# Optimization experiments

Measured on AMD Instinct MI355X. Metric: run time of the kernel, lower is better.

The kernel has to match this reference:

```python
import jax, jax.numpy as jnp
import numpy as np

NUM_CATEGORIES = 72
TEMPERATURE = 0.07
SEGMENT_WEIGHT = 10.0
MISSING_CATEGORIES = (13, 53, 61)
EPS = 1e-12
NEG_INF = -1e30


def setup_inputs() -> dict:
    key = jax.random.key(0)
    k1, k2 = jax.random.split(key)
    B, N, D = 4, 262144, 32
    embeddings = jax.random.normal(k1, (B, N, D), dtype=jnp.float32)
    segment_labels = jax.random.randint(k2, (B, N), 0, NUM_CATEGORIES, dtype=jnp.int64)
    return {"embeddings": embeddings, "segment_labels": segment_labels}


def _l2norm(x):
    return x / jnp.maximum(jnp.linalg.norm(x, axis=-1, keepdims=True), EPS)


def reference(embeddings, segment_labels):
    C = NUM_CATEGORIES
    missing = jnp.zeros((C,), dtype=bool).at[jnp.array(MISSING_CATEGORIES)].set(True)
    valid = segment_labels >= 0                      # [B,N]
    labels = jnp.clip(segment_labels, 0, C - 1)      # safe indices
    emb_n = _l2norm(embeddings)                      # [B,N,D]

    def per_batch(e, lab, v):
        w = v.astype(e.dtype)                                        # [N]
        counts = jax.ops.segment_sum(w, lab, num_segments=C)         # [C]
        sums = jax.ops.segment_sum(e * w[:, None], lab, num_segments=C)  # [C,D]
        protos = _l2norm(sums / jnp.maximum(counts, 1.0)[:, None])   # [C,D]
        present = (counts > 0) & (~missing)                          # [C]
        # similarity over all categories, mask absent/missing prototypes
        sim = jnp.einsum('nd,cd->nc', e, protos) / TEMPERATURE       # [N,C]
        logits = jnp.where(present[None, :], sim, NEG_INF)
        logp = jax.nn.log_softmax(logits, axis=-1)
        nll = -jnp.take_along_axis(logp, lab[:, None], axis=1)[:, 0]  # [N]
        keep = (v & (~missing[lab])).astype(e.dtype)                  # ignore_index=-100 analogue
        return jnp.sum(nll * keep) / jnp.maximum(jnp.sum(keep), 1.0)

    losses = jax.vmap(per_batch)(emb_n, labels, valid)  # [B]
    segment_loss = jnp.mean(losses)                     # segment_count == B here
    return SEGMENT_WEIGHT * segment_loss
```

## Files before the change

kernel.cpp:

```cpp
#include <hip/hip_runtime.h>
#include <hip/hip_bf16.h>

#define NCAT 72
#define NCATP 80
#define DIM 32
#define BNUM 4
#define TEMP_INV (1.0f / 0.07f)
#define SEG_W 10.0f

#define WS_SUMS 0
#define WS_CNTS 9216
#define WS_PROT 9504
#define WS_NABS 19744
#define WS_LOSS 19748
#define WS_KEEP 19752
#define WS_TOTAL 19756

typedef __attribute__((ext_vector_type(8))) short short8v;
typedef __attribute__((ext_vector_type(4))) float f32x4;

__device__ __forceinline__ bool is_missing(int c) {
    return (c == 13) | (c == 53) | (c == 61);
}

__device__ __forceinline__ short f2bf_hi(float f, float* hi_f) {
    unsigned u = __float_as_uint(f);
    unsigned r = u + 0x7FFFu + ((u >> 16) & 1u);
    *hi_f = __uint_as_float(r & 0xFFFF0000u);
    return (short)(r >> 16);
}
__device__ __forceinline__ short f2bf(float f) {
    unsigned u = __float_as_uint(f);
    unsigned r = u + 0x7FFFu + ((u >> 16) & 1u);
    return (short)(r >> 16);
}

template <int BPB>
__global__ __launch_bounds__(256) void k_accum(const float* __restrict__ emb,
                                               const int* __restrict__ lab,
                                               float* __restrict__ ws, int Nb) {
    __shared__ float s_acc[4][NCAT][DIM];
    __shared__ float s_cnt[4][NCAT];
    const int t = threadIdx.x;
    const int b = blockIdx.x / BPB;
    const int blk = blockIdx.x % BPB;
    const int w = t >> 6;
    const int g = (t >> 3) & 7;
    const int sub = t & 7;
    const int pofs = t >> 3;

    for (int i = t; i < 4 * NCAT * DIM; i += 256) ((float*)s_acc)[i] = 0.f;
    for (int i = t; i < 4 * NCAT; i += 256) ((float*)s_cnt)[i] = 0.f;
    __syncthreads();

    float* accw = &s_acc[w][0][0];
    const float* eb = emb + (size_t)b * Nb * DIM;
    const int* lb = lab + (size_t)b * Nb;

    int p = blk * 32 + pofs;
    int l_cur = lb[p];
    float4 v_cur = ((const float4*)(eb + (size_t)p * DIM))[sub];

    for (int p0 = blk * 32; p0 < Nb; p0 += BPB * 32) {
        const int pn = p0 + BPB * 32 + pofs;
        int l_nxt = -1;
        float4 v_nxt = make_float4(0.f, 0.f, 0.f, 0.f);
        if (pn < Nb) {
            l_nxt = lb[pn];
            v_nxt = ((const float4*)(eb + (size_t)pn * DIM))[sub];
        }

        float ss = v_cur.x * v_cur.x + v_cur.y * v_cur.y +
                   v_cur.z * v_cur.z + v_cur.w * v_cur.w;
        ss += __shfl_xor(ss, 1);
        ss += __shfl_xor(ss, 2);
        ss += __shfl_xor(ss, 4);
        const float inv = 1.0f / fmaxf(sqrtf(ss), 1e-12f);
        const bool valid = (l_cur >= 0);
        const int lc = min(max(l_cur, 0), NCAT - 1);
        float4 u;
        u.x = v_cur.x * inv; u.y = v_cur.y * inv;
        u.z = v_cur.z * inv; u.w = v_cur.w * inv;

        if (valid && sub == 0) unsafeAtomicAdd(&s_cnt[w][lc], 1.0f);

        float* rowp = accw + lc * DIM + sub * 4;
        #pragma unroll
        for (int k = 0; k < 8; k++) {
            if (g == k && valid) {
                float4* r4 = (float4*)rowp;
                float4 o = *r4;
                o.x += u.x; o.y += u.y; o.z += u.z; o.w += u.w;
                *r4 = o;
            }
            __builtin_amdgcn_sched_barrier(0);
        }

        l_cur = l_nxt;
        v_cur = v_nxt;
    }
    __syncthreads();

    float* gs = ws + WS_SUMS + b * NCAT * DIM;
    const float* sa = (const float*)s_acc;
    for (int i = t; i < NCAT * DIM; i += 256) {
        float val = sa[i] + sa[NCAT * DIM + i] +
                    sa[2 * NCAT * DIM + i] + sa[3 * NCAT * DIM + i];
        if (val != 0.f) unsafeAtomicAdd(&gs[i], val);
    }
    if (t < NCAT) {
        float c = s_cnt[0][t] + s_cnt[1][t] + s_cnt[2][t] + s_cnt[3][t];
        if (c != 0.f) unsafeAtomicAdd(ws + WS_CNTS + b * NCAT + t, c);
    }
}

__global__ __launch_bounds__(256) void k_proto(float* __restrict__ ws) {
    const int b = blockIdx.x;
    __shared__ float s_np;
    if (threadIdx.x == 0) s_np = 0.f;
    __syncthreads();
    const float* gs = ws + WS_SUMS + b * NCAT * DIM;
    const float* gc = ws + WS_CNTS + b * NCAT;
    float* gp = ws + WS_PROT + b * NCATP * DIM;
    const int dd = threadIdx.x & 31;
    const int r0 = threadIdx.x >> 5;
    for (int c = r0; c < NCAT; c += 8) {
        float cnt = gc[c];
        float val = gs[c * DIM + dd] / fmaxf(cnt, 1.0f);
        float ss = val * val;
        #pragma unroll
        for (int m = 16; m >= 1; m >>= 1) ss += __shfl_xor(ss, m);
        float inv = 1.0f / fmaxf(sqrtf(ss), 1e-12f);
        const bool present = (cnt > 0.f) && !is_missing(c);
        gp[c * DIM + dd] = present ? val * inv : 0.f;
        if (dd == 0) unsafeAtomicAdd(&s_np, present ? 1.f : 0.f);
    }
    __syncthreads();
    if (threadIdx.x == 0) ws[WS_NABS + b] = (float)NCATP - s_np;
}

__device__ __forceinline__ void point_group(
    int pt, const float* __restrict__ eb, const int* __restrict__ lb,
    const float* __restrict__ pp, const short8v phi[5], const short8v plo[5],
    float nabs, int sub, float& lacc, float& kacc)
{
    const float LOG2E = 1.4426950408889634f;
    const int l = lb[pt];
    const int lc = min(max(l, 0), NCAT - 1);

    const float4* ep = (const float4*)(eb + (size_t)pt * DIM + sub * 8);
    float4 a0 = ep[0], a1 = ep[1];

    float ss = a0.x * a0.x + a0.y * a0.y + a0.z * a0.z + a0.w * a0.w +
               a1.x * a1.x + a1.y * a1.y + a1.z * a1.z + a1.w * a1.w;
    ss += __shfl_xor(ss, 16);
    ss += __shfl_xor(ss, 32);
    const float sca = (TEMP_INV * LOG2E) / fmaxf(sqrtf(ss), 1e-12f);
    a0.x *= sca; a0.y *= sca; a0.z *= sca; a0.w *= sca;
    a1.x *= sca; a1.y *= sca; a1.z *= sca; a1.w *= sca;

    const float4* qk = (const float4*)(pp + lc * DIM + sub * 8);
    float4 q0 = qk[0], q1 = qk[1];
    float dl = q0.x * a0.x + q0.y * a0.y + q0.z * a0.z + q0.w * a0.w +
               q1.x * a1.x + q1.y * a1.y + q1.z * a1.z + q1.w * a1.w;
    dl += __shfl_xor(dl, 16);
    dl += __shfl_xor(dl, 32);

    const bool keep = (l >= 0) && !is_missing(lc);

    float ea[8] = {a0.x, a0.y, a0.z, a0.w, a1.x, a1.y, a1.z, a1.w};
    short8v ehi, elo;
    #pragma unroll
    for (int j = 0; j < 8; j++) {
        float hf;
        ehi[j] = f2bf_hi(ea[j], &hf);
        elo[j] = f2bf(ea[j] - hf);
    }

    float s = 0.f;
    #pragma unroll
    for (int n = 0; n < 5; n++) {
        f32x4 acc = {0.f, 0.f, 0.f, 0.f};
        acc = __builtin_amdgcn_mfma_f32_16x16x32_bf16(phi[n], ehi, acc, 0, 0, 0);
        acc = __builtin_amdgcn_mfma_f32_16x16x32_bf16(plo[n], ehi, acc, 0, 0, 0);
        acc = __builtin_amdgcn_mfma_f32_16x16x32_bf16(phi[n], elo, acc, 0, 0, 0);
        s += __builtin_amdgcn_exp2f(acc[0]) + __builtin_amdgcn_exp2f(acc[1]) +
             __builtin_amdgcn_exp2f(acc[2]) + __builtin_amdgcn_exp2f(acc[3]);
    }
    s += __shfl_xor(s, 16);
    s += __shfl_xor(s, 32);
    s -= nabs;
    const float cl = __builtin_amdgcn_logf(s);
    if (keep && sub == 0) {
        lacc += cl - dl;
        kacc += 1.f;
    }
}

template <int BPB>
__global__ __launch_bounds__(256, 4) void k_loss(const float* __restrict__ emb,
                                                 const int* __restrict__ lab,
                                                 const float* __restrict__ protos,
                                                 const float* __restrict__ nabsp,
                                                 float* __restrict__ lossout,
                                                 int Nb) {
    __shared__ float s_red[8];
    const int b = blockIdx.x / BPB;
    const int blk = blockIdx.x % BPB;
    const int t = threadIdx.x;
    const int lane = t & 63;
    const int wave = t >> 6;
    const int lid = lane & 15;
    const int sub = lane >> 4;

    const float* pp = protos + b * NCATP * DIM;
    const float nabs = nabsp[b];
    const float* eb = emb + (size_t)b * Nb * DIM;
    const int* lb = lab + (size_t)b * Nb;
    const float LN2 = 0.6931471805599453f;

    short8v phi[5], plo[5];
    #pragma unroll
    for (int n = 0; n < 5; n++) {
        const int cat = n * 16 + lid;
        const float4* qk = (const float4*)(pp + cat * DIM + sub * 8);
        float4 q0 = qk[0], q1 = qk[1];
        float qa[8] = {q0.x, q0.y, q0.z, q0.w, q1.x, q1.y, q1.z, q1.w};
        #pragma unroll
        for (int j = 0; j < 8; j++) {
            float hf;
            phi[n][j] = f2bf_hi(qa[j], &hf);
            plo[n][j] = f2bf(qa[j] - hf);
        }
    }

    float lacc = 0.f, kacc = 0.f;

    #pragma unroll 1
    for (int p0 = (blk * 4 + wave) * 32; p0 < Nb; p0 += BPB * 4 * 32) {
        point_group(p0 + lid,      eb, lb, pp, phi, plo, nabs, sub, lacc, kacc);
        point_group(p0 + 16 + lid, eb, lb, pp, phi, plo, nabs, sub, lacc, kacc);
    }

    #pragma unroll
    for (int m = 32; m >= 1; m >>= 1) {
        lacc += __shfl_xor(lacc, m);
        kacc += __shfl_xor(kacc, m);
    }
    if (lane == 0) {
        s_red[wave] = lacc;
        s_red[4 + wave] = kacc;
    }
    __syncthreads();
    if (t == 0) {
        float a = s_red[0] + s_red[1] + s_red[2] + s_red[3];
        float k = s_red[4] + s_red[5] + s_red[6] + s_red[7];
        unsafeAtomicAdd(lossout + b, LN2 * a);
        unsafeAtomicAdd(lossout + BNUM + b, k);
    }
}

__global__ void k_final(const float* __restrict__ ws, float* __restrict__ out) {
    if (threadIdx.x == 0 && blockIdx.x == 0) {
        float s = 0.f;
        for (int b = 0; b < BNUM; b++) {
            float l = ws[WS_LOSS + b];
            float k = ws[WS_KEEP + b];
            s += l / fmaxf(k, 1.0f);
        }
        out[0] = SEG_W * (s / BNUM);
    }
}

extern "C" void kernel_launch(void* const* d_in, const int* in_sizes, int n_in,
                              void* d_out, int out_size, void* d_ws, size_t ws_size,
                              hipStream_t stream) {
    const float* emb = (const float*)d_in[0];
    const int* lab = (const int*)d_in[1];
    float* ws = (float*)d_ws;
    float* out = (float*)d_out;
    const int total_pts = in_sizes[1];
    const int Nb = total_pts / BNUM;

    hipMemsetAsync(d_ws, 0, WS_TOTAL * sizeof(float), stream);
    constexpr int BPB_ACC = 256;
    constexpr int BPB_LOSS = 256;
    k_accum<BPB_ACC><<<dim3(BNUM * BPB_ACC), dim3(256), 0, stream>>>(emb, lab, ws, Nb);
    k_proto<<<dim3(BNUM), dim3(256), 0, stream>>>(ws);
    k_loss<BPB_LOSS><<<dim3(BNUM * BPB_LOSS), dim3(256), 0, stream>>>(
        emb, lab, ws + WS_PROT, ws + WS_NABS, ws + WS_LOSS, Nb);
    k_final<<<1, 64, 0, stream>>>(ws, out);
}
```

Baseline: 136.5 us.

## Accumulate prototype sums with one-hot MFMA instead of LDS scatter

The per-category sum and count scatter in the accumulation kernel is recast as a one-hot bf16 MFMA product. A hi/lo bf16 split keeps precision, and the results accumulate in registers instead of serialized LDS read-modify-writes. All four waves of a block process the same 32 points, which quadruples the accumulation work. Because sums and counts scale by the same factor and prototypes are renormalized, the result stays correct. The change also lowers the accumulation grid to 192 blocks per batch with a 3-blocks-per-CU launch bound, and unrolls the loss loop to four point groups per iteration.

```diff
diff --git a/kernel.cpp b/kernel.cpp
--- a/kernel.cpp
+++ b/kernel.cpp
@@ -36,81 +36,114 @@
 }
 
 template <int BPB>
-__global__ __launch_bounds__(256) void k_accum(const float* __restrict__ emb,
-                                               const int* __restrict__ lab,
-                                               float* __restrict__ ws, int Nb) {
-    __shared__ float s_acc[4][NCAT][DIM];
-    __shared__ float s_cnt[4][NCAT];
+__global__ __launch_bounds__(256, 3) void k_accum(const float* __restrict__ emb,
+                                                  const int* __restrict__ lab,
+                                                  float* __restrict__ ws, int Nb) {
+    __shared__ float s_s[4][NCATP][DIM];
+    __shared__ float s_c[4][NCATP];
     const int t = threadIdx.x;
     const int b = blockIdx.x / BPB;
     const int blk = blockIdx.x % BPB;
     const int w = t >> 6;
-    const int g = (t >> 3) & 7;
-    const int sub = t & 7;
-    const int pofs = t >> 3;
-
-    for (int i = t; i < 4 * NCAT * DIM; i += 256) ((float*)s_acc)[i] = 0.f;
-    for (int i = t; i < 4 * NCAT; i += 256) ((float*)s_cnt)[i] = 0.f;
-    __syncthreads();
-
-    float* accw = &s_acc[w][0][0];
+    const int lane = t & 63;
+    const int lid = lane & 15;
+    const int kc = lane >> 4;
+
     const float* eb = emb + (size_t)b * Nb * DIM;
     const int* lb = lab + (size_t)b * Nb;
 
-    int p = blk * 32 + pofs;
-    int l_cur = lb[p];
-    float4 v_cur = ((const float4*)(eb + (size_t)p * DIM))[sub];
-
+    f32x4 accs[5][2];
+    f32x4 accc[5];
+    #pragma unroll
+    for (int n = 0; n < 5; n++) {
+        accs[n][0] = (f32x4){0.f, 0.f, 0.f, 0.f};
+        accs[n][1] = (f32x4){0.f, 0.f, 0.f, 0.f};
+        accc[n] = (f32x4){0.f, 0.f, 0.f, 0.f};
+    }
+    short8v bone;
+    #pragma unroll
+    for (int j = 0; j < 8; j++) bone[j] = (short)0x3F80;
+
+    #pragma unroll 1
     for (int p0 = blk * 32; p0 < Nb; p0 += BPB * 32) {
-        const int pn = p0 + BPB * 32 + pofs;
-        int l_nxt = -1;
-        float4 v_nxt = make_float4(0.f, 0.f, 0.f, 0.f);
-        if (pn < Nb) {
-            l_nxt = lb[pn];
-            v_nxt = ((const float4*)(eb + (size_t)pn * DIM))[sub];
-        }
-
-        float ss = v_cur.x * v_cur.x + v_cur.y * v_cur.y +
-                   v_cur.z * v_cur.z + v_cur.w * v_cur.w;
-        ss += __shfl_xor(ss, 1);
-        ss += __shfl_xor(ss, 2);
-        ss += __shfl_xor(ss, 4);
-        const float inv = 1.0f / fmaxf(sqrtf(ss), 1e-12f);
-        const bool valid = (l_cur >= 0);
-        const int lc = min(max(l_cur, 0), NCAT - 1);
-        float4 u;
-        u.x = v_cur.x * inv; u.y = v_cur.y * inv;
-        u.z = v_cur.z * inv; u.w = v_cur.w * inv;
-
-        if (valid && sub == 0) unsafeAtomicAdd(&s_cnt[w][lc], 1.0f);
-
-        float* rowp = accw + lc * DIM + sub * 4;
-        #pragma unroll
-        for (int k = 0; k < 8; k++) {
-            if (g == k && valid) {
-                float4* r4 = (float4*)rowp;
-                float4 o = *r4;
-                o.x += u.x; o.y += u.y; o.z += u.z; o.w += u.w;
-                *r4 = o;
-            }
-            __builtin_amdgcn_sched_barrier(0);
-        }
-
-        l_cur = l_nxt;
-        v_cur = v_nxt;
+        const int pb = p0 + kc * 8;
+        int lcl[8];
+        int hi4[8];
+        bool va[8];
+        #pragma unroll
+        for (int j = 0; j < 8; j++) {
+            const int l = lb[pb + j];
+            va[j] = (l >= 0);
+            lcl[j] = min(max(l, 0), NCAT - 1);
+            hi4[j] = lcl[j] >> 4;
+        }
+        float v0[8], v1[8];
+        #pragma unroll
+        for (int j = 0; j < 8; j++) {
+            const float* r = eb + (size_t)(pb + j) * DIM;
+            v0[j] = r[lid];
+            v1[j] = r[lid + 16];
+        }
+        float ssp[8];
+        #pragma unroll
+        for (int j = 0; j < 8; j++) ssp[j] = v0[j] * v0[j] + v1[j] * v1[j];
+        #pragma unroll
+        for (int m = 1; m <= 8; m <<= 1) {
+            #pragma unroll
+            for (int j = 0; j < 8; j++) ssp[j] += __shfl_xor(ssp[j], m);
+        }
+        short8v b0h, b0l, b1h, b1l;
+        #pragma unroll
+        for (int j = 0; j < 8; j++) {
+            const float inv = 1.0f / fmaxf(sqrtf(ssp[j]), 1e-12f);
+            float h;
+            const float x0 = v0[j] * inv;
+            b0h[j] = f2bf_hi(x0, &h); b0l[j] = f2bf(x0 - h);
+            const float x1 = v1[j] * inv;
+            b1h[j] = f2bf_hi(x1, &h); b1l[j] = f2bf(x1 - h);
+        }
+        short hit[8];
+        #pragma unroll
+        for (int j = 0; j < 8; j++)
+            hit[j] = (va[j] && ((lcl[j] & 15) == lid)) ? (short)0x3F80 : (short)0;
+
+        #pragma unroll
+        for (int n = 0; n < 5; n++) {
+            short8v a;
+            #pragma unroll
+            for (int j = 0; j < 8; j++) a[j] = (hi4[j] == n) ? hit[j] : (short)0;
+            accs[n][0] = __builtin_amdgcn_mfma_f32_16x16x32_bf16(a, b0h, accs[n][0], 0, 0, 0);
+            accs[n][0] = __builtin_amdgcn_mfma_f32_16x16x32_bf16(a, b0l, accs[n][0], 0, 0, 0);
+            accs[n][1] = __builtin_amdgcn_mfma_f32_16x16x32_bf16(a, b1h, accs[n][1], 0, 0, 0);
+            accs[n][1] = __builtin_amdgcn_mfma_f32_16x16x32_bf16(a, b1l, accs[n][1], 0, 0, 0);
+            accc[n]    = __builtin_amdgcn_mfma_f32_16x16x32_bf16(a, bone, accc[n], 0, 0, 0);
+        }
+    }
+
+    #pragma unroll
+    for (int n = 0; n < 5; n++) {
+        const int cat = n * 16 + kc * 4;
+        #pragma unroll
+        for (int r = 0; r < 4; r++) {
+            s_s[w][cat + r][lid] = accs[n][0][r];
+            s_s[w][cat + r][lid + 16] = accs[n][1][r];
+        }
+        if (lid == 0) {
+            #pragma unroll
+            for (int r = 0; r < 4; r++) s_c[w][cat + r] = accc[n][r];
+        }
     }
     __syncthreads();
 
     float* gs = ws + WS_SUMS + b * NCAT * DIM;
-    const float* sa = (const float*)s_acc;
     for (int i = t; i < NCAT * DIM; i += 256) {
-        float val = sa[i] + sa[NCAT * DIM + i] +
-                    sa[2 * NCAT * DIM + i] + sa[3 * NCAT * DIM + i];
+        const int c = i >> 5, d = i & 31;
+        float val = s_s[0][c][d] + s_s[1][c][d] + s_s[2][c][d] + s_s[3][c][d];
         if (val != 0.f) unsafeAtomicAdd(&gs[i], val);
     }
     if (t < NCAT) {
-        float c = s_cnt[0][t] + s_cnt[1][t] + s_cnt[2][t] + s_cnt[3][t];
-        if (c != 0.f) unsafeAtomicAdd(ws + WS_CNTS + b * NCAT + t, c);
+        float cc = s_c[0][t] + s_c[1][t] + s_c[2][t] + s_c[3][t];
+        if (cc != 0.f) unsafeAtomicAdd(ws + WS_CNTS + b * NCAT + t, cc);
     }
 }
 
@@ -237,9 +270,11 @@
     float lacc = 0.f, kacc = 0.f;
 
     #pragma unroll 1
-    for (int p0 = (blk * 4 + wave) * 32; p0 < Nb; p0 += BPB * 4 * 32) {
+    for (int p0 = (blk * 4 + wave) * 64; p0 < Nb; p0 += BPB * 4 * 64) {
         point_group(p0 + lid,      eb, lb, pp, phi, plo, nabs, sub, lacc, kacc);
         point_group(p0 + 16 + lid, eb, lb, pp, phi, plo, nabs, sub, lacc, kacc);
+        point_group(p0 + 32 + lid, eb, lb, pp, phi, plo, nabs, sub, lacc, kacc);
+        point_group(p0 + 48 + lid, eb, lb, pp, phi, plo, nabs, sub, lacc, kacc);
     }
 
     #pragma unroll
@@ -283,7 +318,7 @@
     const int Nb = total_pts / BNUM;
 
     hipMemsetAsync(d_ws, 0, WS_TOTAL * sizeof(float), stream);
-    constexpr int BPB_ACC = 256;
+    constexpr int BPB_ACC = 192;
     constexpr int BPB_LOSS = 256;
     k_accum<BPB_ACC><<<dim3(BNUM * BPB_ACC), dim3(256), 0, stream>>>(emb, lab, ws, Nb);
     k_proto<<<dim3(BNUM), dim3(256), 0, stream>>>(ws);
```

Result: slower. 229.4 us (+68.0%).
